# Performance work log

Measured on AMD Instinct MI355X. Metric: run time of the kernel, lower is better.

Reference implementation:

```python
import jax, jax.numpy as jnp
import numpy as np

B, N, F_NODE = 16, 48, 5
H1, H2 = 32, 64
D_ATT = H2 * 3  # 192


def setup_inputs() -> dict:
    rng = np.random.default_rng(0)
    n_nodes = B * N
    # complete graph per batch element; each directed pair appears with class 0 and class 1,
    # ordered by (src, dst, class) so that filtering src>dst leaves a sorted list where
    # consecutive rows are the (class0, class1) pair of the same undirected edge.
    i, j = np.meshgrid(np.arange(N), np.arange(N), indexing="ij")
    m = i != j
    pi = np.repeat(i[m], 2)
    pj = np.repeat(j[m], 2)
    cls = np.tile(np.array([0.0, 1.0], np.float32), N * (N - 1))
    offs = np.arange(B)[:, None] * N
    src = (pi[None] + offs).ravel()
    dst = (pj[None] + offs).ravel()
    edges = jnp.asarray(np.stack([src, dst]).astype(np.int64))
    w = rng.random(src.shape[0]).astype(np.float32)
    edge_attr = jnp.asarray(np.stack([w, np.tile(cls, B)], axis=1))
    x = jnp.asarray(rng.standard_normal((n_nodes, F_NODE)).astype(np.float32))
    detector_labels = jnp.ones((n_nodes,), bool)
    batch_labels = jnp.asarray(np.repeat(np.arange(B), N).astype(np.int64))

    def lin(k_out, k_in):
        s = 1.0 / np.sqrt(k_in)
        return (jnp.asarray(rng.uniform(-s, s, (k_out, k_in)).astype(np.float32)),
                jnp.asarray(rng.uniform(-s, s, (k_out,)).astype(np.float32)))

    W_we, b_we = lin(1, 3)
    Wrel1, brel1 = lin(H1, F_NODE); Wroot1, _ = lin(H1, F_NODE)
    Wrel2, brel2 = lin(H2, H1);     Wroot2, _ = lin(H2, H1)
    W_ee, b_ee = lin(H2, 3)
    W_qkv, b_qkv = lin(3 * D_ATT, D_ATT)
    W_in, b_in = lin(3 * D_ATT, D_ATT)
    W_out, b_out = lin(D_ATT, D_ATT)
    W_o, b_o = lin(1, D_ATT)
    return dict(x=x, edges=edges, edge_attr=edge_attr,
                detector_labels=detector_labels, batch_labels=batch_labels,
                W_we=W_we, b_we=b_we, Wrel1=Wrel1, brel1=brel1, Wroot1=Wroot1,
                Wrel2=Wrel2, brel2=brel2, Wroot2=Wroot2,
                W_ee=W_ee, b_ee=b_ee, W_qkv=W_qkv, b_qkv=b_qkv,
                W_in=W_in, b_in=b_in, W_out=W_out, b_out=b_out,
                W_o=W_o, b_o=b_o)


def _graph_conv(x, src, dst, w, Wrel, brel, Wroot, n_nodes):
    # pyg GraphConv: lin_rel(sum_{j->i} e_ji * x_j) + lin_root(x_i)
    msg = x[src] * w  # w: [E,1] scalar edge weight
    agg = jax.ops.segment_sum(msg, dst, num_segments=n_nodes)
    return agg @ Wrel.T + brel + x @ Wroot.T


def reference(x, edges, edge_attr, detector_labels, batch_labels,
              W_we, b_we, Wrel1, brel1, Wroot1, Wrel2, brel2, Wroot2,
              W_ee, b_ee, W_qkv, b_qkv, W_in, b_in, W_out, b_out, W_o, b_o):
    n_nodes = x.shape[0]
    E = edges.shape[1]
    src, dst = edges[0], edges[1]
    # edge weight embedding from (weight, one_hot(class))
    c = jax.nn.one_hot(edge_attr[:, 1].astype(jnp.int32), 2, dtype=x.dtype)
    w = jax.nn.relu(jnp.concatenate([edge_attr[:, :1], c], -1) @ W_we.T + b_we)  # [E,1]
    x = jax.nn.relu(_graph_conv(x, src, dst, w, Wrel1, brel1, Wroot1, n_nodes))
    x = jax.nn.relu(_graph_conv(x, src, dst, w, Wrel2, brel2, Wroot2, n_nodes))
    # keep one direction (src > dst): construction guarantees exactly E//2 kept, already sorted
    keep = jnp.nonzero(src > dst, size=E // 2)[0]
    srcK, dstK, ea = src[keep], dst[keep], edge_attr[keep]
    c = jax.nn.one_hot(ea[:, 1].astype(jnp.int32), 2, dtype=x.dtype)
    wK = jax.nn.relu(jnp.concatenate([ea[:, :1], c], -1) @ W_ee.T + b_ee)  # [Ek,H2]
    feat = jnp.concatenate([x[srcK], wK, x[dstK]], -1)  # [Ek, 3*H2]
    # equal-size graphs -> unbatch + pad_sequence == reshape (no padding)
    S = feat.shape[0] // B
    feat = feat.reshape(B, S, -1)
    e_src = srcK.reshape(B, S)
    e_dst = dstK.reshape(B, S)
    classes = ea[:, 1].reshape(B, S, 1)
    pad_mask = e_src == e_dst  # all False (no ragged padding here)
    # SelfAttention: extra qkv projection, then 1-head MultiheadAttention
    qkv = feat @ W_qkv.T + b_qkv
    q, k, v = jnp.split(qkv, 3, -1)
    Wq, Wk, Wv = jnp.split(W_in, 3, 0)
    bq, bk, bv = jnp.split(b_in, 3, 0)
    q = q @ Wq.T + bq; k = k @ Wk.T + bk; v = v @ Wv.T + bv
    scores = jnp.einsum("bqd,bkd->bqk", q, k) / jnp.sqrt(jnp.asarray(q.shape[-1], q.dtype))
    scores = jnp.where(pad_mask[:, None, :], -jnp.inf, scores)
    attn = jax.nn.softmax(scores, -1)
    feat = jnp.einsum("bqk,bkd->bqd", attn, v) @ W_out.T + b_out
    # SplitSyndromes with all-True detector_labels keeps every edge (identity)
    logit = feat @ W_o.T + b_o  # [B,S,1]
    pair = jnp.concatenate([logit[:, ::2], logit[:, 1::2]], -1)   # [B,S/2,2]
    cls2 = jnp.concatenate([classes[:, ::2], classes[:, 1::2]], -1)
    min_inds = jnp.argmin(pair, axis=2, keepdims=True)
    ef = jnp.take_along_axis(pair, min_inds, 2)   # min values, [B,S/2,1]
    ec = jnp.take_along_axis(cls2, min_inds, 2)
    e4s = jnp.stack([e_src[:, ::2], e_src[:, 1::2]], -1)  # [B,S/2,2]
    e4t = jnp.stack([e_dst[:, ::2], e_dst[:, 1::2]], -1)
    out_src = jnp.take_along_axis(e4s, min_inds, -1)
    out_dst = jnp.take_along_axis(e4t, min_inds, -1)
    out_edges = jnp.concatenate([out_src, out_dst], -1)
    return out_edges, ef, ec
```

## Files before the change

kernel.cpp:

```cpp
#include <hip/hip_runtime.h>
#include <hip/hip_bf16.h>

typedef __hip_bfloat16 bf16;
typedef __attribute__((ext_vector_type(8))) short short8;
typedef __attribute__((ext_vector_type(16))) float float16v;
typedef __attribute__((ext_vector_type(2))) float float2v;

#define B_     16
#define N_     48
#define NODES  768
#define PAIRS  2256
#define EK     36096
#define S_     2256
#define SH     1128
#define D_     192
#define KITERS 71
#define QTILES 71
#define QSCALE 0.10411754f

__device__ __forceinline__ float bf(const bf16* p, int i) { return __bfloat162float(p[i]); }
__device__ __forceinline__ float u2f(unsigned short u) {
    return __uint_as_float(((unsigned int)u) << 16);
}
__device__ __forceinline__ float sanitize(float v) {
    if (v > -1e4f && v < 1e4f) return v;
    if (v >= 1e4f) return 1e4f;
    if (v <= -1e4f) return -1e4f;
    return 0.f;
}

__global__ __launch_bounds__(256) void stage1_kernel(
    const bf16* edge_attr, const bf16* W_we, const bf16* b_we, const bf16* x,
    const bf16* Wrel1, const bf16* brel1, const bf16* Wroot1,
    const bf16* Wrel2, const bf16* brel2, const bf16* Wroot2,
    const bf16* W_o, const bf16* b_o, const bf16* W_out, const bf16* b_out,
    const bf16* W_in, const bf16* b_in, const bf16* b_qkv, const bf16* W_qkv,
    float* x2out, float* wo_eff, float* bq_eff, float* bk_eff, float* bv_eff, float* sc,
    float* WqT, float* WkT, bf16* W2b) {
    int blk = blockIdx.x, tid = threadIdx.x;
    if (blk < 16) {
        int b = blk;
        __shared__ float s_ws[N_ * N_];
        __shared__ float s_x[N_ * 5], s_agg1[N_ * 5];
        __shared__ float s_x1[N_ * 32], s_agg2[N_ * 32];
        float we0 = bf(W_we, 0), we1 = bf(W_we, 1), we2 = bf(W_we, 2), bw = bf(b_we, 0);
        for (int idx = tid; idx < N_ * N_; idx += 256) {
            int i = idx / N_, j = idx % N_;
            float v = 0.f;
            if (i != j) {
                int p = i * 47 + (j < i ? j : j - 1);
                int e = (b * PAIRS + p) * 2;
                float w0 = fmaxf(we0 * bf(edge_attr, (e + 0) * 2) + we1 + bw, 0.f);
                float w1 = fmaxf(we0 * bf(edge_attr, (e + 1) * 2) + we2 + bw, 0.f);
                v = w0 + w1;
            }
            s_ws[idx] = v;
        }
        for (int idx = tid; idx < N_ * 5; idx += 256) s_x[idx] = bf(x, b * N_ * 5 + idx);
        __syncthreads();
        if (tid < 240) {
            int j = tid / 5, f = tid % 5;
            float a = 0.f;
            for (int i = 0; i < N_; i++) a += s_ws[i * N_ + j] * s_x[i * 5 + f];
            s_agg1[tid] = a;
        }
        __syncthreads();
        for (int o = tid; o < N_ * 32; o += 256) {
            int j = o >> 5, h = o & 31;
            float a = bf(brel1, h);
            for (int f = 0; f < 5; f++)
                a += bf(Wrel1, h * 5 + f) * s_agg1[j * 5 + f] +
                     bf(Wroot1, h * 5 + f) * s_x[j * 5 + f];
            s_x1[o] = fmaxf(a, 0.f);
        }
        __syncthreads();
        for (int o = tid; o < N_ * 32; o += 256) {
            int j = o >> 5, h = o & 31;
            float a = 0.f;
            for (int i = 0; i < N_; i++) a += s_ws[i * N_ + j] * s_x1[i * 32 + h];
            s_agg2[o] = a;
        }
        __syncthreads();
        for (int o = tid; o < N_ * 64; o += 256) {
            int j = o >> 6, h2 = o & 63;
            float a = bf(brel2, h2);
            for (int h1 = 0; h1 < 32; h1++)
                a += bf(Wrel2, h2 * 32 + h1) * s_agg2[j * 32 + h1] +
                     bf(Wroot2, h2 * 32 + h1) * s_x1[j * 32 + h1];
            x2out[(b * N_ + j) * 64 + h2] = fmaxf(a, 0.f);
        }
    } else if (blk < 209) {
        int a = blk - 16;
        int wave = tid >> 6, lane = tid & 63;
        float partial = 0.f;
        if (a < 192) {
            if (wave == 0) {
                for (int m = lane; m < 192; m += 64)
                    partial += bf(W_o, m) * bf(W_out, m * 192 + a);
            } else {
                int row = (wave - 1) * 192 + a;
                for (int m = lane; m < 192; m += 64)
                    partial += bf(W_in, row * 192 + m) * bf(b_qkv, (wave - 1) * 192 + m);
            }
        } else if (wave == 0) {
            for (int m = lane; m < 192; m += 64) partial += bf(W_o, m) * bf(b_out, m);
        }
        for (int off = 32; off; off >>= 1) partial += __shfl_xor(partial, off, 64);
        if (lane == 0) {
            if (a < 192) {
                if (wave == 0) wo_eff[a] = partial;
                else if (wave == 1) bq_eff[a] = partial + bf(b_in, a);
                else if (wave == 2) bk_eff[a] = partial + bf(b_in, 192 + a);
                else bv_eff[a] = partial + bf(b_in, 384 + a);
            } else if (wave == 0) sc[1] = partial + bf(b_o, 0);
        }
    } else {
        int idx = (blk - 209) * 256 + tid;
        if (idx < D_ * D_) {
            int a = idx / D_, c = idx % D_;
            float acc = 0.f;
            for (int m = 0; m < D_; m++) acc += bf(W_in, a * D_ + m) * bf(W_qkv, m * D_ + c);
            WqT[c * D_ + a] = acc;
            if (c >= 64 && c < 128) W2b[a * 64 + (c - 64)] = __float2bfloat16(acc);
        } else {
            int t = idx - D_ * D_, a = t / D_, c = t % D_;
            float acc = 0.f;
            for (int m = 0; m < D_; m++)
                acc += bf(W_in, (D_ + a) * D_ + m) * bf(W_qkv, (D_ + m) * D_ + c);
            WkT[c * D_ + a] = acc;
            if (c >= 64 && c < 128) W2b[(192 + a) * 64 + (c - 64)] = __float2bfloat16(acc);
        }
    }
}

__global__ __launch_bounds__(256) void stage2_kernel(
    const bf16* W_in, const float* wo_eff, const float* bv_eff,
    const float* x2, const float* WqT, const float* WkT,
    const float* bq_eff, const float* bk_eff,
    float* t_m, float* sc, float* Tq1, float* Tq3, float* Tk1, float* Tk3) {
    int blk = blockIdx.x, tid = threadIdx.x;
    if (blk < 49) {
        int w = blk * 4 + (tid >> 6);
        int lane = tid & 63;
        float partial = 0.f;
        if (w < 192) {
            for (int aa = lane; aa < 192; aa += 64)
                partial += wo_eff[aa] * bf(W_in, (384 + aa) * 192 + w);
        } else if (w == 192) {
            for (int aa = lane; aa < 192; aa += 64) partial += wo_eff[aa] * bv_eff[aa];
        }
        for (int off = 32; off; off >>= 1) partial += __shfl_xor(partial, off, 64);
        if (lane == 0) {
            if (w < 192) t_m[w] = partial;
            else if (w == 192) sc[0] = partial;
        }
    } else {
        int n = blk - 49;
        __shared__ float sx[64];
        if (tid < 64) sx[tid] = x2[n * 64 + tid];
        __syncthreads();
        if (tid < D_) {
            int a = tid;
            float q1 = bq_eff[a], q3 = 0.f, k1 = bk_eff[a], k3 = 0.f;
            for (int c = 0; c < 64; c++) {
                float xv = sx[c];
                q1 += WqT[c * D_ + a] * xv;
                q3 += WqT[(128 + c) * D_ + a] * xv;
                k1 += WkT[c * D_ + a] * xv;
                k3 += WkT[(128 + c) * D_ + a] * xv;
            }
            Tq1[n * D_ + a] = q1; Tq3[n * D_ + a] = q3;
            Tk1[n * D_ + a] = k1; Tk3[n * D_ + a] = k3;
        }
    }
}

__global__ __launch_bounds__(256) void wvl_kernel(const bf16* W_qkv, const float* t_m,
                                                  float* wvl) {
    int w = blockIdx.x * 4 + (threadIdx.x >> 6);
    int lane = threadIdx.x & 63;
    if (w >= 192) return;
    float partial = 0.f;
    for (int m = lane; m < 192; m += 64)
        partial += t_m[m] * bf(W_qkv, (384 + m) * 192 + w);
    for (int off = 32; off; off >>= 1) partial += __shfl_xor(partial, off, 64);
    if (lane == 0) wvl[w] = partial;
}

__global__ __launch_bounds__(256) void qkvmid_kernel(
    const bf16* edge_attr, const bf16* W_ee, const bf16* b_ee, const bf16* W2b,
    const float* wvl, const float* sc, const float* x2,
    const float* Tq1, const float* Tq3, const float* Tk1, const float* Tk3,
    bf16* Q, bf16* K, float* vl) {
    __shared__ short s_wk[32 * 72];
    __shared__ float s_wvl[192];
    __shared__ int s_ni[32], s_nj[32];
    __shared__ float s_wraw[32], s_cls[32];
    int tid = threadIdx.x, base = blockIdx.x * 32;
    int wave = tid >> 6, lane = tid & 63;
    int l5 = lane & 31, h5 = lane >> 5;

    short8 bfr[3][4];
    #pragma unroll
    for (int tt = 0; tt < 3; tt++) {
        int ta = wave + tt * 4;
        const short* wrow = (const short*)W2b + (ta * 32 + l5) * 64;
        #pragma unroll
        for (int kc = 0; kc < 4; kc++)
            bfr[tt][kc] = *(const short8*)(wrow + kc * 16 + h5 * 8);
    }

    if (tid < 192) s_wvl[tid] = wvl[tid];
    if (tid < 32) {
        int kk_g = base + tid;
        int b = kk_g / S_, kk = kk_g % S_;
        int q = kk >> 1, cls = kk & 1;
        int i = (int)((1.0f + sqrtf(8.0f * (float)q + 1.0f)) * 0.5f);
        while (i * (i - 1) / 2 > q) --i;
        while ((i + 1) * i / 2 <= q) ++i;
        int j = q - i * (i - 1) / 2;
        s_ni[tid] = b * N_ + i; s_nj[tid] = b * N_ + j;
        int e = (b * PAIRS + i * 47 + j) * 2 + cls;
        s_wraw[tid] = bf(edge_attr, e * 2);
        s_cls[tid] = (float)cls;
    }
    __syncthreads();
    for (int idx = tid; idx < 32 * 64; idx += 256) {
        int t = idx >> 6, h = idx & 63;
        int cls = (int)s_cls[t];
        float v = bf(W_ee, h * 3) * s_wraw[t] + bf(W_ee, h * 3 + 1 + cls) + bf(b_ee, h);
        bf16 bv = __float2bfloat16(fmaxf(v, 0.f));
        s_wk[t * 72 + h] = *reinterpret_cast<short*>(&bv);
    }
    __syncthreads();

    short8 af[4];
    #pragma unroll
    for (int kc = 0; kc < 4; kc++)
        af[kc] = *(const short8*)&s_wk[l5 * 72 + kc * 16 + h5 * 8];

    int tl[16], niv[16], njv[16];
    #pragma unroll
    for (int r = 0; r < 16; r++) {
        int t = (r & 3) + 8 * (r >> 2) + 4 * h5;
        tl[r] = t; niv[r] = s_ni[t]; njv[r] = s_nj[t];
    }

    #pragma unroll
    for (int tt = 0; tt < 3; tt++) {
        int ta = wave + tt * 4;
        bool isq = ta < 6;
        int ag = (isq ? ta : ta - 6) * 32 + l5;
        float16v c;
        #pragma unroll
        for (int r = 0; r < 16; r++) c[r] = 0.f;
        #pragma unroll
        for (int kc = 0; kc < 4; kc++)
            c = __builtin_amdgcn_mfma_f32_32x32x16_bf16(af[kc], bfr[tt][kc], c, 0, 0, 0);
        const float* T1 = isq ? Tq1 : Tk1;
        const float* T3 = isq ? Tq3 : Tk3;
        bf16* Out = isq ? Q : K;
        #pragma unroll
        for (int r = 0; r < 16; r++) {
            float v = c[r] + T1[niv[r] * D_ + ag] + T3[njv[r] * D_ + ag];
            if (isq) v *= QSCALE;
            Out[(long)(base + tl[r]) * D_ + ag] = __float2bfloat16(v);
        }
    }
    {
        int t = tid >> 3, g = tid & 7;
        const float* xi = &x2[s_ni[t] * 64];
        const float* xj = &x2[s_nj[t] * 64];
        float v = 0.f;
        #pragma unroll
        for (int hh = 0; hh < 8; hh++) {
            int h = g * 8 + hh;
            v += s_wvl[h] * xi[h] + s_wvl[128 + h] * xj[h] +
                 s_wvl[64 + h] * u2f((unsigned short)s_wk[t * 72 + h]);
        }
        v += __shfl_xor(v, 1, 64);
        v += __shfl_xor(v, 2, 64);
        v += __shfl_xor(v, 4, 64);
        if (g == 0) vl[base + t] = v + sc[0];
    }
}

__global__ __launch_bounds__(512) void attn_kernel(const bf16* Q, const bf16* K,
                                                   const float* vl, float* part) {
    int x = blockIdx.x;
    int rr = x & 7, rest = x >> 3;
    int hi = rest >= 72;
    int b = rr + 8 * hi;
    int s = rest - 72 * hi;
    int chunk = s / 9, qg = s % 9;
    int tid = threadIdx.x;
    int wave = tid >> 6, lane = tid & 63;
    int n5 = lane & 31, h5 = lane >> 5;
    int qt = qg * 8 + wave;
    bool qvalid = qt < QTILES;
    int t0 = chunk * 9;
    int nit = (chunk == 7) ? 8 : 9;

    __shared__ short s_k[2][32 * 200];
    __shared__ float s_vl[2][32];

    int row0 = tid / 24, cc0 = tid % 24;
    int c1 = tid + 512;
    int row1 = c1 / 24, cc1 = c1 % 24;
    bool has1 = tid < 256;

    short8 qf[12];
    {
        int qrow = b * S_ + qt * 32 + n5;
        if (qrow > B_ * S_ - 1) qrow = B_ * S_ - 1;
        const short* qp = (const short*)Q + (long)qrow * D_;
        #pragma unroll
        for (int kc = 0; kc < 12; kc++) qf[kc] = *(const short8*)(qp + kc * 16 + h5 * 8);
    }

    float lr[16], ar[16];
    #pragma unroll
    for (int r = 0; r < 16; r++) { lr[r] = 0.f; ar[r] = 0.f; }

    uint4 p0, p1; float pv = 0.f;
    {
        int key = t0 * 32 + row0;
        int gk = b * S_ + (key < S_ ? key : S_ - 1);
        p0 = *(const uint4*)((const short*)K + (long)gk * D_ + cc0 * 8);
        if (has1) {
            int key1 = t0 * 32 + row1;
            int gk1 = b * S_ + (key1 < S_ ? key1 : S_ - 1);
            p1 = *(const uint4*)((const short*)K + (long)gk1 * D_ + cc1 * 8);
        }
        if (tid < 32) {
            int key2 = t0 * 32 + tid;
            pv = (key2 < S_) ? vl[b * S_ + key2] : 0.f;
        }
    }

    for (int k = 0; k < nit; ++k) {
        int it = t0 + k;
        int buf = k & 1;
        *(uint4*)&s_k[buf][row0 * 200 + cc0 * 8] = p0;
        if (has1) *(uint4*)&s_k[buf][row1 * 200 + cc1 * 8] = p1;
        if (tid < 32) s_vl[buf][tid] = pv;
        if (k + 1 < nit) {
            int it1 = it + 1;
            int key = it1 * 32 + row0;
            int gk = b * S_ + (key < S_ ? key : S_ - 1);
            p0 = *(const uint4*)((const short*)K + (long)gk * D_ + cc0 * 8);
            if (has1) {
                int key1 = it1 * 32 + row1;
                int gk1 = b * S_ + (key1 < S_ ? key1 : S_ - 1);
                p1 = *(const uint4*)((const short*)K + (long)gk1 * D_ + cc1 * 8);
            }
            if (tid < 32) {
                int key2 = it1 * 32 + tid;
                pv = (key2 < S_) ? vl[b * S_ + key2] : 0.f;
            }
        }
        __syncthreads();
        const short* kb = s_k[buf];
        float16v c;
        #pragma unroll
        for (int r = 0; r < 16; r++) c[r] = 0.f;
        #pragma unroll
        for (int kc = 0; kc < 12; kc++) {
            short8 bfr = *(const short8*)(kb + n5 * 200 + kc * 16 + h5 * 8);
            c = __builtin_amdgcn_mfma_f32_32x32x16_bf16(qf[kc], bfr, c, 0, 0, 0);
        }
        float vlv = s_vl[buf][n5];
        if (it != KITERS - 1) {
            #pragma unroll
            for (int r = 0; r < 16; r++) {
                float p = __builtin_amdgcn_exp2f(c[r]);
                lr[r] += p;
                ar[r] += p * vlv;
            }
        } else {
            bool kv = n5 < 16;
            #pragma unroll
            for (int r = 0; r < 16; r++) {
                float p = kv ? __builtin_amdgcn_exp2f(c[r]) : 0.f;
                lr[r] += p;
                ar[r] += p * vlv;
            }
        }
    }

    if (qvalid) {
        #pragma unroll
        for (int r = 0; r < 16; r++) {
            float l = lr[r], a = ar[r];
            #pragma unroll
            for (int off = 1; off < 32; off <<= 1) {
                l += __shfl_xor(l, off, 64);
                a += __shfl_xor(a, off, 64);
            }
            if (n5 == 0) {
                int qrow = qt * 32 + (r & 3) + 8 * (r >> 2) + 4 * h5;
                if (qrow < S_) {
                    float2v pv2 = {l, a};
                    *(float2v*)&part[((long)(b * S_ + qrow) * 8 + chunk) * 2] = pv2;
                }
            }
        }
    }
}

__global__ __launch_bounds__(256) void final_kernel(const float* part, const float* sc,
                                                    float* out) {
    int idx = blockIdx.x * 256 + threadIdx.x;
    if (idx >= B_ * SH) return;
    int b = idx / SH, p = idx % SH;
    int i = (int)((1.0f + sqrtf(8.0f * (float)p + 1.0f)) * 0.5f);
    while (i * (i - 1) / 2 > p) --i;
    while ((i + 1) * i / 2 <= p) ++i;
    int j = p - i * (i - 1) / 2;
    float co = sc[1];
    float lg[2];
    #pragma unroll
    for (int t = 0; t < 2; t++) {
        long g = (long)b * S_ + 2 * p + t;
        float l = 0.f, a = 0.f;
        #pragma unroll
        for (int c = 0; c < 8; c++) {
            float2v pc = *(const float2v*)&part[(g * 8 + c) * 2];
            l += pc.x;
            a += pc.y;
        }
        lg[t] = sanitize(a / l + co);
    }
    int ind = (lg[1] < lg[0]) ? 1 : 0;
    float ef = ind ? lg[1] : lg[0];
    out[(b * SH + p) * 2 + 0] = (float)(b * N_ + i);
    out[(b * SH + p) * 2 + 1] = (float)(b * N_ + j);
    out[2 * B_ * SH + idx] = ef;
    out[2 * B_ * SH + B_ * SH + idx] = (float)ind;
}

extern "C" void kernel_launch(void* const* d_in, const int* in_sizes, int n_in,
                              void* d_out, int out_size, void* d_ws, size_t ws_size,
                              hipStream_t stream) {
    const bf16* x         = (const bf16*)d_in[0];
    const bf16* edge_attr = (const bf16*)d_in[2];
    const bf16* W_we   = (const bf16*)d_in[5];
    const bf16* b_we   = (const bf16*)d_in[6];
    const bf16* Wrel1  = (const bf16*)d_in[7];
    const bf16* brel1  = (const bf16*)d_in[8];
    const bf16* Wroot1 = (const bf16*)d_in[9];
    const bf16* Wrel2  = (const bf16*)d_in[10];
    const bf16* brel2  = (const bf16*)d_in[11];
    const bf16* Wroot2 = (const bf16*)d_in[12];
    const bf16* W_ee   = (const bf16*)d_in[13];
    const bf16* b_ee   = (const bf16*)d_in[14];
    const bf16* W_qkv  = (const bf16*)d_in[15];
    const bf16* b_qkv  = (const bf16*)d_in[16];
    const bf16* W_in   = (const bf16*)d_in[17];
    const bf16* b_in   = (const bf16*)d_in[18];
    const bf16* W_out  = (const bf16*)d_in[19];
    const bf16* b_out  = (const bf16*)d_in[20];
    const bf16* W_o    = (const bf16*)d_in[21];
    const bf16* b_o    = (const bf16*)d_in[22];

    float* w = (float*)d_ws;
    float* WqT    = w;
    float* WkT    = WqT + 36864;
    float* t_m    = WkT + 36864;
    float* bq_eff = t_m + 192;
    float* bk_eff = bq_eff + 192;
    float* bv_eff = bk_eff + 192;
    float* wo_eff = bv_eff + 192;
    float* wvl    = wo_eff + 192;
    float* sc     = wvl + 192;
    float* x2     = sc + 64;
    float* vl     = x2 + 49152;
    float* part   = vl + 36096;
    bf16*  Q      = (bf16*)(part + 577536);
    bf16*  K      = Q + (long)EK * D_;
    bf16*  W2b    = K + (long)EK * D_;
    float* Tq1    = (float*)(W2b + 384 * 64);
    float* Tq3    = Tq1 + NODES * D_;
    float* Tk1    = Tq3 + NODES * D_;
    float* Tk3    = Tk1 + NODES * D_;

    stage1_kernel<<<497, 256, 0, stream>>>(edge_attr, W_we, b_we, x, Wrel1, brel1, Wroot1,
                                           Wrel2, brel2, Wroot2, W_o, b_o, W_out, b_out,
                                           W_in, b_in, b_qkv, W_qkv,
                                           x2, wo_eff, bq_eff, bk_eff, bv_eff, sc,
                                           WqT, WkT, W2b);
    stage2_kernel<<<817, 256, 0, stream>>>(W_in, wo_eff, bv_eff, x2, WqT, WkT,
                                           bq_eff, bk_eff, t_m, sc, Tq1, Tq3, Tk1, Tk3);
    wvl_kernel<<<48, 256, 0, stream>>>(W_qkv, t_m, wvl);
    qkvmid_kernel<<<EK / 32, 256, 0, stream>>>(edge_attr, W_ee, b_ee, W2b, wvl, sc, x2,
                                               Tq1, Tq3, Tk1, Tk3, Q, K, vl);
    attn_kernel<<<1152, 512, 0, stream>>>(Q, K, vl, part);
    final_kernel<<<(B_ * SH + 255) / 256, 256, 0, stream>>>(part, sc, (float*)d_out);
}
```

Before: 239.8 us.

## Load attention K tiles directly from global and fold wvl kernel into stage2

```diff
diff --git a/kernel.cpp b/kernel.cpp
--- a/kernel.cpp
+++ b/kernel.cpp
@@ -134,28 +134,37 @@
 }
 
 __global__ __launch_bounds__(256) void stage2_kernel(
-    const bf16* W_in, const float* wo_eff, const float* bv_eff,
+    const bf16* W_in, const bf16* W_qkv, const float* wo_eff, const float* bv_eff,
     const float* x2, const float* WqT, const float* WkT,
     const float* bq_eff, const float* bk_eff,
-    float* t_m, float* sc, float* Tq1, float* Tq3, float* Tk1, float* Tk3) {
+    float* wvl, float* sc, float* Tq1, float* Tq3, float* Tk1, float* Tk3) {
     int blk = blockIdx.x, tid = threadIdx.x;
-    if (blk < 49) {
-        int w = blk * 4 + (tid >> 6);
-        int lane = tid & 63;
-        float partial = 0.f;
-        if (w < 192) {
-            for (int aa = lane; aa < 192; aa += 64)
-                partial += wo_eff[aa] * bf(W_in, (384 + aa) * 192 + w);
-        } else if (w == 192) {
-            for (int aa = lane; aa < 192; aa += 64) partial += wo_eff[aa] * bv_eff[aa];
-        }
-        for (int off = 32; off; off >>= 1) partial += __shfl_xor(partial, off, 64);
-        if (lane == 0) {
-            if (w < 192) t_m[w] = partial;
-            else if (w == 192) sc[0] = partial;
+    if (blk == 0) {
+        if (tid < 64) {
+            float partial = 0.f;
+            for (int aa = tid; aa < 192; aa += 64) partial += wo_eff[aa] * bv_eff[aa];
+            for (int off = 32; off; off >>= 1) partial += __shfl_xor(partial, off, 64);
+            if (tid == 0) sc[0] = partial;
+        }
+    } else if (blk < 193) {
+        int w = blk - 1;
+        __shared__ float s_tm[192];
+        if (tid < 192) {
+            float tm = 0.f;
+            for (int aa = 0; aa < 192; aa++)
+                tm += wo_eff[aa] * bf(W_in, (384 + aa) * 192 + tid);
+            s_tm[tid] = tm;
+        }
+        __syncthreads();
+        if (tid < 64) {
+            float partial = 0.f;
+            for (int m = tid; m < 192; m += 64)
+                partial += s_tm[m] * bf(W_qkv, (384 + m) * 192 + w);
+            for (int off = 32; off; off >>= 1) partial += __shfl_xor(partial, off, 64);
+            if (tid == 0) wvl[w] = partial;
         }
     } else {
-        int n = blk - 49;
+        int n = blk - 193;
         __shared__ float sx[64];
         if (tid < 64) sx[tid] = x2[n * 64 + tid];
         __syncthreads();
@@ -173,18 +182,6 @@
             Tk1[n * D_ + a] = k1; Tk3[n * D_ + a] = k3;
         }
     }
-}
-
-__global__ __launch_bounds__(256) void wvl_kernel(const bf16* W_qkv, const float* t_m,
-                                                  float* wvl) {
-    int w = blockIdx.x * 4 + (threadIdx.x >> 6);
-    int lane = threadIdx.x & 63;
-    if (w >= 192) return;
-    float partial = 0.f;
-    for (int m = lane; m < 192; m += 64)
-        partial += t_m[m] * bf(W_qkv, (384 + m) * 192 + w);
-    for (int off = 32; off; off >>= 1) partial += __shfl_xor(partial, off, 64);
-    if (lane == 0) wvl[w] = partial;
 }
 
 __global__ __launch_bounds__(256) void qkvmid_kernel(
@@ -285,29 +282,21 @@
     }
 }
 
-__global__ __launch_bounds__(512) void attn_kernel(const bf16* Q, const bf16* K,
+__global__ __launch_bounds__(256) void attn_kernel(const bf16* Q, const bf16* K,
                                                    const float* vl, float* part) {
     int x = blockIdx.x;
     int rr = x & 7, rest = x >> 3;
-    int hi = rest >= 72;
+    int hi = rest >= 144;
     int b = rr + 8 * hi;
-    int s = rest - 72 * hi;
-    int chunk = s / 9, qg = s % 9;
+    int s = rest - 144 * hi;
+    int chunk = s / 18, qg = s % 18;
     int tid = threadIdx.x;
     int wave = tid >> 6, lane = tid & 63;
     int n5 = lane & 31, h5 = lane >> 5;
-    int qt = qg * 8 + wave;
+    int qt = qg * 4 + wave;
     bool qvalid = qt < QTILES;
     int t0 = chunk * 9;
     int nit = (chunk == 7) ? 8 : 9;
-
-    __shared__ short s_k[2][32 * 200];
-    __shared__ float s_vl[2][32];
-
-    int row0 = tid / 24, cc0 = tid % 24;
-    int c1 = tid + 512;
-    int row1 = c1 / 24, cc1 = c1 % 24;
-    bool has1 = tid < 256;
 
     short8 qf[12];
     {
@@ -322,54 +311,24 @@
     #pragma unroll
     for (int r = 0; r < 16; r++) { lr[r] = 0.f; ar[r] = 0.f; }
 
-    uint4 p0, p1; float pv = 0.f;
-    {
-        int key = t0 * 32 + row0;
-        int gk = b * S_ + (key < S_ ? key : S_ - 1);
-        p0 = *(const uint4*)((const short*)K + (long)gk * D_ + cc0 * 8);
-        if (has1) {
-            int key1 = t0 * 32 + row1;
-            int gk1 = b * S_ + (key1 < S_ ? key1 : S_ - 1);
-            p1 = *(const uint4*)((const short*)K + (long)gk1 * D_ + cc1 * 8);
-        }
-        if (tid < 32) {
-            int key2 = t0 * 32 + tid;
-            pv = (key2 < S_) ? vl[b * S_ + key2] : 0.f;
-        }
-    }
+    const short* Kb = (const short*)K + (long)b * S_ * D_;
+    const float* vlb = vl + b * S_;
 
     for (int k = 0; k < nit; ++k) {
         int it = t0 + k;
-        int buf = k & 1;
-        *(uint4*)&s_k[buf][row0 * 200 + cc0 * 8] = p0;
-        if (has1) *(uint4*)&s_k[buf][row1 * 200 + cc1 * 8] = p1;
-        if (tid < 32) s_vl[buf][tid] = pv;
-        if (k + 1 < nit) {
-            int it1 = it + 1;
-            int key = it1 * 32 + row0;
-            int gk = b * S_ + (key < S_ ? key : S_ - 1);
-            p0 = *(const uint4*)((const short*)K + (long)gk * D_ + cc0 * 8);
-            if (has1) {
-                int key1 = it1 * 32 + row1;
-                int gk1 = b * S_ + (key1 < S_ ? key1 : S_ - 1);
-                p1 = *(const uint4*)((const short*)K + (long)gk1 * D_ + cc1 * 8);
-            }
-            if (tid < 32) {
-                int key2 = it1 * 32 + tid;
-                pv = (key2 < S_) ? vl[b * S_ + key2] : 0.f;
-            }
-        }
-        __syncthreads();
-        const short* kb = s_k[buf];
+        int row = it * 32 + n5;
+        int rowc = row < S_ ? row : S_ - 1;
+        const short* kp = Kb + (long)rowc * D_ + h5 * 8;
+        short8 bfr[12];
+        #pragma unroll
+        for (int kc = 0; kc < 12; kc++) bfr[kc] = *(const short8*)(kp + kc * 16);
+        float vlv = vlb[rowc];
         float16v c;
         #pragma unroll
         for (int r = 0; r < 16; r++) c[r] = 0.f;
         #pragma unroll
-        for (int kc = 0; kc < 12; kc++) {
-            short8 bfr = *(const short8*)(kb + n5 * 200 + kc * 16 + h5 * 8);
-            c = __builtin_amdgcn_mfma_f32_32x32x16_bf16(qf[kc], bfr, c, 0, 0, 0);
-        }
-        float vlv = s_vl[buf][n5];
+        for (int kc = 0; kc < 12; kc++)
+            c = __builtin_amdgcn_mfma_f32_32x32x16_bf16(qf[kc], bfr[kc], c, 0, 0, 0);
         if (it != KITERS - 1) {
             #pragma unroll
             for (int r = 0; r < 16; r++) {
@@ -466,8 +425,7 @@
     float* w = (float*)d_ws;
     float* WqT    = w;
     float* WkT    = WqT + 36864;
-    float* t_m    = WkT + 36864;
-    float* bq_eff = t_m + 192;
+    float* bq_eff = WkT + 36864;
     float* bk_eff = bq_eff + 192;
     float* bv_eff = bk_eff + 192;
     float* wo_eff = bv_eff + 192;
@@ -489,11 +447,10 @@
                                            W_in, b_in, b_qkv, W_qkv,
                                            x2, wo_eff, bq_eff, bk_eff, bv_eff, sc,
                                            WqT, WkT, W2b);
-    stage2_kernel<<<817, 256, 0, stream>>>(W_in, wo_eff, bv_eff, x2, WqT, WkT,
-                                           bq_eff, bk_eff, t_m, sc, Tq1, Tq3, Tk1, Tk3);
-    wvl_kernel<<<48, 256, 0, stream>>>(W_qkv, t_m, wvl);
+    stage2_kernel<<<961, 256, 0, stream>>>(W_in, W_qkv, wo_eff, bv_eff, x2, WqT, WkT,
+                                           bq_eff, bk_eff, wvl, sc, Tq1, Tq3, Tk1, Tk3);
     qkvmid_kernel<<<EK / 32, 256, 0, stream>>>(edge_attr, W_ee, b_ee, W2b, wvl, sc, x2,
                                                Tq1, Tq3, Tk1, Tk3, Q, K, vl);
-    attn_kernel<<<1152, 512, 0, stream>>>(Q, K, vl, part);
+    attn_kernel<<<2304, 256, 0, stream>>>(Q, K, vl, part);
     final_kernel<<<(B_ * SH + 255) / 256, 256, 0, stream>>>(part, sc, (float*)d_out);
 }
```

Result: slower. 300.7 us (+25.4%).
